# Kernel tuning notes

Measured on AMD Instinct MI355X. Metric: run time of the kernel, lower is better.

Reference implementation:

```python
import jax, jax.numpy as jnp
import numpy as np

B, N, D_IN, D, H, L, K = 64, 1024, 16, 256, 4, 3, 64
DH = D // H
DFF = 4 * D
TAU = 0.5


def setup_inputs() -> dict:
    key = jax.random.key(0)
    ks = jax.random.split(key, 24)
    nrm = lambda k, s: jax.random.normal(k, s, jnp.float32) * 0.02
    u = jax.random.uniform(ks[1], (B, N), jnp.float32, 1e-6, 1.0 - 1e-6)
    return {
        "x": jax.random.normal(ks[0], (B, N, D_IN), jnp.float32),
        "gumbel": -jnp.log(-jnp.log(u)),
        "emb_W": nrm(ks[2], (D_IN, D)), "emb_b": jnp.zeros((D,), jnp.float32),
        "Wq": nrm(ks[3], (L, D, D)), "Wk": nrm(ks[4], (L, D, D)),
        "Wv": nrm(ks[5], (L, D, D)), "Wo": nrm(ks[6], (L, D, D)),
        "ln1_g": jnp.ones((L, D), jnp.float32), "ln1_b": jnp.zeros((L, D), jnp.float32),
        "ln2_g": jnp.ones((L, D), jnp.float32), "ln2_b": jnp.zeros((L, D), jnp.float32),
        "ffn_W1": nrm(ks[7], (L, D, DFF)), "ffn_b1": jnp.zeros((L, DFF), jnp.float32),
        "ffn_W2": nrm(ks[8], (L, DFF, D)), "ffn_b2": jnp.zeros((L, D), jnp.float32),
        "sha_Wq": nrm(ks[9], (D, D)), "sha_Wk": nrm(ks[10], (D, D)),
        "alloc_W1": nrm(ks[11], (D, D)), "alloc_b1": jnp.zeros((D,), jnp.float32),
        "alloc_W2": nrm(ks[12], (D, N)), "alloc_b2": jnp.zeros((N,), jnp.float32),
    }


def _ln(x, g, b):
    m = x.mean(-1, keepdims=True)
    v = ((x - m) ** 2).mean(-1, keepdims=True)
    return (x - m) * jax.lax.rsqrt(v + 1e-5) * g + b


def reference(x, gumbel, emb_W, emb_b, Wq, Wk, Wv, Wo, ln1_g, ln1_b, ln2_g, ln2_b,
              ffn_W1, ffn_b1, ffn_W2, ffn_b2, sha_Wq, sha_Wk,
              alloc_W1, alloc_b1, alloc_W2, alloc_b2):
    h = x @ emb_W + emb_b  # [B,N,D]
    scale = 1.0 / jnp.sqrt(jnp.float32(DH))
    for i in range(L):  # fixed small layer count
        q = (h @ Wq[i]).reshape(B, N, H, DH)
        k = (h @ Wk[i]).reshape(B, N, H, DH)
        v = (h @ Wv[i]).reshape(B, N, H, DH)
        attn = jax.nn.softmax(jnp.einsum('bqhd,bkhd->bhqk', q, k) * scale, axis=-1)
        o = jnp.einsum('bhqk,bkhd->bqhd', attn, v).reshape(B, N, D) @ Wo[i]
        h = _ln(h + o, ln1_g[i], ln1_b[i])
        f = jax.nn.relu(h @ ffn_W1[i] + ffn_b1[i]) @ ffn_W2[i] + ffn_b2[i]
        h = _ln(h + f, ln2_g[i], ln2_b[i])
    h_mean = h.mean(axis=1)  # [B,D]
    qv = h_mean @ sha_Wq  # [B,D]
    kv = h @ sha_Wk       # [B,N,D]
    scores = jnp.einsum('bd,bnd->bn', qv, kv) / jnp.sqrt(jnp.float32(D))  # [B,N]
    weights = jax.nn.softmax((scores + gumbel) / TAU, axis=-1)  # gumbel-softmax, hard=False
    topk_vals, topk_idx = jax.lax.top_k(weights, K)
    logits = jax.nn.relu(h_mean @ alloc_W1 + alloc_b1) @ alloc_W2 + alloc_b2  # [B,N]
    alloc = jax.nn.softmax(logits, axis=-1)
    sel = jnp.take_along_axis(alloc, topk_idx, axis=1)  # [B,K]
    sel = sel / (sel.sum(axis=1, keepdims=True) + 1e-12)
    return weights, topk_idx, sel
```

## Files before the change

kernel.cpp:

```cpp
#include <hip/hip_runtime.h>
#include <math.h>

#define BB   64
#define NN   1024
#define DIN  16
#define DD   256
#define HH   4
#define LL   3
#define DHH  64
#define DFF2 1024
#define KSEL 64

__global__ __launch_bounds__(256) void embed_kernel(
    const float* __restrict__ x, const float* __restrict__ W,
    const float* __restrict__ bias, float* __restrict__ h)
{
  __shared__ float xs[4][DIN];
  const int t = threadIdx.x, w = t >> 6, lane = t & 63;
  const size_t row = (size_t)blockIdx.x * 4 + w;
  if (lane < DIN) xs[w][lane] = x[row * DIN + lane];
  __syncthreads();
#pragma unroll
  for (int j = 0; j < 4; ++j) {
    const int col = lane + j * 64;
    float acc = bias[col];
#pragma unroll
    for (int kk = 0; kk < DIN; ++kk) acc = fmaf(xs[w][kk], W[kk * DD + col], acc);
    h[row * DD + col] = acc;
  }
}

__global__ __launch_bounds__(256) void gemm128_kernel(
    const float* __restrict__ A, int lda,
    const float* __restrict__ Bm, int ldb,
    float* C, int ldc,
    const float* __restrict__ bias,
    const float* res, int ldres,
    int Kk, int relu, int accum)
{
  __shared__ __align__(16) float As[8][132];
  __shared__ __align__(16) float Bs[8][132];
  const int t = threadIdx.x;
  const int tx = t & 15, ty = t >> 4;
  const size_t row0 = (size_t)blockIdx.y * 128;
  const size_t col0 = (size_t)blockIdx.x * 128;
  const int arow = t >> 1, aq = (t & 1) * 4;
  const int brow = t >> 5, bcq = t & 31;
  const int bphys = ((bcq >> 1) | ((bcq & 1) << 4)) * 4;
  float acc[8][8] = {};
  const float* Aptr = A + (row0 + arow) * lda + aq;
  const float* Bptr = Bm + (size_t)brow * ldb + col0 + bcq * 4;

  for (int k0 = 0; k0 < Kk; k0 += 8) {
    const float4 av = *(const float4*)(Aptr + k0);
    const float4 bv = *(const float4*)(Bptr + (size_t)k0 * ldb);
    As[aq + 0][arow] = av.x; As[aq + 1][arow] = av.y;
    As[aq + 2][arow] = av.z; As[aq + 3][arow] = av.w;
    *(float4*)&Bs[brow][bphys] = bv;
    __syncthreads();
#pragma unroll
    for (int kk = 0; kk < 8; ++kk) {
      const float4 a0 = *(const float4*)&As[kk][ty * 8];
      const float4 a1 = *(const float4*)&As[kk][ty * 8 + 4];
      const float4 b0 = *(const float4*)&Bs[kk][tx * 4];
      const float4 b1 = *(const float4*)&Bs[kk][tx * 4 + 64];
      const float aa[8] = {a0.x, a0.y, a0.z, a0.w, a1.x, a1.y, a1.z, a1.w};
      const float bb2[8] = {b0.x, b0.y, b0.z, b0.w, b1.x, b1.y, b1.z, b1.w};
#pragma unroll
      for (int i = 0; i < 8; ++i)
#pragma unroll
        for (int j = 0; j < 8; ++j)
          acc[i][j] = fmaf(aa[i], bb2[j], acc[i][j]);
    }
    __syncthreads();
  }
#pragma unroll
  for (int i = 0; i < 8; ++i) {
    const size_t r = row0 + ty * 8 + i;
    float* cp = C + r * (size_t)ldc + col0 + tx * 8;
    const float* rp = res ? res + r * (size_t)ldres + col0 + tx * 8 : nullptr;
#pragma unroll
    for (int j = 0; j < 8; ++j) {
      const size_t c = col0 + tx * 8 + j;
      float v = acc[i][j];
      if (bias) v += bias[c];
      if (rp)   v += rp[j];
      if (relu) v = fmaxf(v, 0.f);
      if (accum) v += cp[j];
      cp[j] = v;
    }
  }
}

#define TOFF(r, cq) ((r) * 68 + 4 * ((cq) ^ (((r) >> 2) & 15)))

__global__ __launch_bounds__(256) void attn_kernel(
    const float* __restrict__ qb, const float* __restrict__ kb,
    const float* __restrict__ vb, float* __restrict__ ob)
{
  __shared__ __align__(16) float Qn[64 * 68];
  __shared__ __align__(16) float KV[64 * 68];
  __shared__ __align__(16) float Pt[64 * 68];
  const int t = threadIdx.x;
  const int tx = t & 15, ty = t >> 4;
  const int qt = blockIdx.x, hh = blockIdx.y, b = blockIdx.z;
  const size_t base = ((size_t)b * NN) * DD + (size_t)hh * DHH;

  const int srow = t >> 4, scq = t & 15;

  {
    const float* qp = qb + base + (size_t)(qt * 64) * DD + scq * 4;
    const float* kp = kb + base + scq * 4;
#pragma unroll
    for (int u = 0; u < 4; ++u) {
      const int r = srow + 16 * u;
      *(float4*)&Qn[TOFF(r, scq)] = *(const float4*)(qp + (size_t)r * DD);
      *(float4*)&KV[TOFF(r, scq)] = *(const float4*)(kp + (size_t)r * DD);
    }
  }

  float S[4][4], O[4][4] = {}, mrun[4], lrun[4] = {};
#pragma unroll
  for (int i = 0; i < 4; ++i) mrun[i] = -1e30f;

  for (int kt = 0; kt < 16; ++kt) {
    __syncthreads();

    float4 vreg[4];
    {
      const float* vp = vb + base + (size_t)(kt * 64) * DD + scq * 4;
#pragma unroll
      for (int u = 0; u < 4; ++u)
        vreg[u] = *(const float4*)(vp + (size_t)(srow + 16 * u) * DD);
    }

#pragma unroll
    for (int i = 0; i < 4; ++i)
#pragma unroll
      for (int j = 0; j < 4; ++j) S[i][j] = 0.f;
#pragma unroll
    for (int dq = 0; dq < 16; ++dq) {
      float4 q4[4], k4[4];
#pragma unroll
      for (int ii = 0; ii < 4; ++ii) q4[ii] = *(const float4*)&Qn[TOFF(4 * ty + ii, dq)];
#pragma unroll
      for (int jj = 0; jj < 4; ++jj) k4[jj] = *(const float4*)&KV[TOFF(4 * tx + jj, dq)];
#pragma unroll
      for (int ii = 0; ii < 4; ++ii)
#pragma unroll
        for (int jj = 0; jj < 4; ++jj)
          S[ii][jj] += q4[ii].x * k4[jj].x + q4[ii].y * k4[jj].y +
                       q4[ii].z * k4[jj].z + q4[ii].w * k4[jj].w;
    }

    float alpha[4];
#pragma unroll
    for (int ii = 0; ii < 4; ++ii) {
      float mt = -1e30f;
#pragma unroll
      for (int jj = 0; jj < 4; ++jj) { S[ii][jj] *= 0.125f; mt = fmaxf(mt, S[ii][jj]); }
#pragma unroll
      for (int off = 1; off < 16; off <<= 1) mt = fmaxf(mt, __shfl_xor(mt, off));
      const float mnew = fmaxf(mrun[ii], mt);
      alpha[ii] = __expf(mrun[ii] - mnew);
      mrun[ii] = mnew;
      float rs = 0.f;
#pragma unroll
      for (int jj = 0; jj < 4; ++jj) { S[ii][jj] = __expf(S[ii][jj] - mnew); rs += S[ii][jj]; }
#pragma unroll
      for (int off = 1; off < 16; off <<= 1) rs += __shfl_xor(rs, off);
      lrun[ii] = lrun[ii] * alpha[ii] + rs;
    }
#pragma unroll
    for (int jj = 0; jj < 4; ++jj) {
      float4 pv = {S[0][jj], S[1][jj], S[2][jj], S[3][jj]};
      *(float4*)&Pt[TOFF(4 * tx + jj, ty)] = pv;
    }

    __syncthreads();

#pragma unroll
    for (int u = 0; u < 4; ++u)
      *(float4*)&KV[TOFF(srow + 16 * u, scq)] = vreg[u];

    float4 kreg[4];
    {
      const int ktn = (kt + 1) & 15;
      const float* kp = kb + base + (size_t)(ktn * 64) * DD + scq * 4;
#pragma unroll
      for (int u = 0; u < 4; ++u)
        kreg[u] = *(const float4*)(kp + (size_t)(srow + 16 * u) * DD);
    }

    __syncthreads();

#pragma unroll
    for (int ii = 0; ii < 4; ++ii)
#pragma unroll
      for (int jj = 0; jj < 4; ++jj) O[ii][jj] *= alpha[ii];
#pragma unroll
    for (int c = 0; c < 64; ++c) {
      const float4 p4 = *(const float4*)&Pt[TOFF(c, ty)];
      const float4 v4 = *(const float4*)&KV[TOFF(c, tx)];
      const float pp[4] = {p4.x, p4.y, p4.z, p4.w};
      const float vv[4] = {v4.x, v4.y, v4.z, v4.w};
#pragma unroll
      for (int ii = 0; ii < 4; ++ii)
#pragma unroll
        for (int jj = 0; jj < 4; ++jj)
          O[ii][jj] = fmaf(pp[ii], vv[jj], O[ii][jj]);
    }

    __syncthreads();

#pragma unroll
    for (int u = 0; u < 4; ++u)
      *(float4*)&KV[TOFF(srow + 16 * u, scq)] = kreg[u];
  }

#pragma unroll
  for (int ii = 0; ii < 4; ++ii) {
    const float inv = 1.f / lrun[ii];
    float4 o4 = {O[ii][0] * inv, O[ii][1] * inv, O[ii][2] * inv, O[ii][3] * inv};
    *(float4*)(ob + base + (size_t)(qt * 64 + 4 * ty + ii) * DD + 4 * tx) = o4;
  }
}

__global__ __launch_bounds__(256) void ln_kernel(
    const float* in, float* out,
    const float* __restrict__ g, const float* __restrict__ bb)
{
  const int t = threadIdx.x, w = t >> 6, lane = t & 63;
  const size_t row = (size_t)blockIdx.x * 4 + w;
  const float4 val = *(const float4*)(in + row * DD + lane * 4);
  float s = val.x + val.y + val.z + val.w;
#pragma unroll
  for (int off = 32; off; off >>= 1) s += __shfl_xor(s, off);
  const float mean = s * (1.f / 256.f);
  const float dx = val.x - mean, dy = val.y - mean, dz = val.z - mean, dw = val.w - mean;
  float ss = dx * dx + dy * dy + dz * dz + dw * dw;
#pragma unroll
  for (int off = 32; off; off >>= 1) ss += __shfl_xor(ss, off);
  const float inv = rsqrtf(ss * (1.f / 256.f) + 1e-5f);
  const float4 g4 = *(const float4*)(g + lane * 4);
  const float4 b4 = *(const float4*)(bb + lane * 4);
  float4 o4;
  o4.x = dx * inv * g4.x + b4.x;
  o4.y = dy * inv * g4.y + b4.y;
  o4.z = dz * inv * g4.z + b4.z;
  o4.w = dw * inv * g4.w + b4.w;
  *(float4*)(out + row * DD + lane * 4) = o4;
}

__global__ __launch_bounds__(256) void rowmean_kernel(
    const float* __restrict__ h, float* __restrict__ hm)
{
  const int t = threadIdx.x, b = blockIdx.x;
  const float* p = h + (size_t)b * NN * DD + t;
  float acc = 0.f;
  for (int n = 0; n < NN; ++n) acc += p[(size_t)n * DD];
  hm[b * DD + t] = acc * (1.f / NN);
}

__global__ __launch_bounds__(256) void final_small_kernel(
    const float* __restrict__ hm, const float* __restrict__ shaWq,
    const float* __restrict__ W1, const float* __restrict__ b1,
    const float* __restrict__ W2, const float* __restrict__ b2,
    float* __restrict__ qv, float* __restrict__ allocp)
{
  __shared__ float hs[256];
  __shared__ float mids[256];
  __shared__ float red[256];
  const int t = threadIdx.x, b = blockIdx.x;
  hs[t] = hm[b * 256 + t];
  __syncthreads();
  float a = 0.f, m2 = b1[t];
  for (int kk = 0; kk < 256; ++kk) {
    const float hv = hs[kk];
    a  = fmaf(hv, shaWq[kk * 256 + t], a);
    m2 = fmaf(hv, W1[kk * 256 + t], m2);
  }
  qv[b * 256 + t] = a;
  mids[t] = fmaxf(m2, 0.f);
  __syncthreads();
  float lg[4];
#pragma unroll
  for (int j = 0; j < 4; ++j) {
    const int n = t + j * 256;
    float acc2 = b2[n];
    for (int kk = 0; kk < 256; ++kk) acc2 = fmaf(mids[kk], W2[kk * 1024 + n], acc2);
    lg[j] = acc2;
  }
  float m = fmaxf(fmaxf(lg[0], lg[1]), fmaxf(lg[2], lg[3]));
  red[t] = m; __syncthreads();
  for (int s2 = 128; s2; s2 >>= 1) { if (t < s2) red[t] = fmaxf(red[t], red[t + s2]); __syncthreads(); }
  m = red[0]; __syncthreads();
  float e[4]; float ls = 0.f;
#pragma unroll
  for (int j = 0; j < 4; ++j) { e[j] = expf(lg[j] - m); ls += e[j]; }
  red[t] = ls; __syncthreads();
  for (int s2 = 128; s2; s2 >>= 1) { if (t < s2) red[t] += red[t + s2]; __syncthreads(); }
  const float invs = 1.f / red[0];
#pragma unroll
  for (int j = 0; j < 4; ++j) allocp[(size_t)b * 1024 + t + j * 256] = e[j] * invs;
}

__global__ __launch_bounds__(256) void scores_kernel(
    const float* __restrict__ qv, const float* __restrict__ kv,
    const float* __restrict__ gum, float* __restrict__ outW,
    float* __restrict__ wcopy)
{
  __shared__ __align__(16) float qs[256];
  __shared__ float sc[1024];
  __shared__ float red[256];
  const int t = threadIdx.x, b = blockIdx.x;
  const int w = t >> 6, lane = t & 63;
  qs[t] = qv[b * 256 + t];
  __syncthreads();
  const float4 myq = *(const float4*)&qs[lane * 4];
  for (int n = w; n < 1024; n += 4) {
    const float4 k4 = *(const float4*)(kv + ((size_t)b * 1024 + n) * 256 + lane * 4);
    float d = myq.x * k4.x + myq.y * k4.y + myq.z * k4.z + myq.w * k4.w;
#pragma unroll
    for (int off = 32; off; off >>= 1) d += __shfl_xor(d, off);
    if (lane == 0) sc[n] = d * (1.f / 16.f);
  }
  __syncthreads();
  float z[4];
#pragma unroll
  for (int j = 0; j < 4; ++j) {
    const int n = t + j * 256;
    z[j] = (sc[n] + gum[(size_t)b * 1024 + n]) * 2.0f;
  }
  float m = fmaxf(fmaxf(z[0], z[1]), fmaxf(z[2], z[3]));
  red[t] = m; __syncthreads();
  for (int s2 = 128; s2; s2 >>= 1) { if (t < s2) red[t] = fmaxf(red[t], red[t + s2]); __syncthreads(); }
  m = red[0]; __syncthreads();
  float e[4]; float ls = 0.f;
#pragma unroll
  for (int j = 0; j < 4; ++j) { e[j] = expf(z[j] - m); ls += e[j]; }
  red[t] = ls; __syncthreads();
  for (int s2 = 128; s2; s2 >>= 1) { if (t < s2) red[t] += red[t + s2]; __syncthreads(); }
  const float invs = 1.f / red[0];
#pragma unroll
  for (int j = 0; j < 4; ++j) {
    const int n = t + j * 256;
    const float wv = e[j] * invs;
    outW[(size_t)b * 1024 + n] = wv;
    wcopy[(size_t)b * 1024 + n] = wv;
  }
}

__global__ __launch_bounds__(256) void topk_kernel(
    const float* __restrict__ wcopy, const float* __restrict__ allocp,
    float* __restrict__ outI, float* __restrict__ outS)
{
  __shared__ float wv[1024];
  __shared__ float rv[4];
  __shared__ int   ri[4];
  __shared__ int   sel[64];
  const int t = threadIdx.x, b = blockIdx.x;
  const int w = t >> 6, lane = t & 63;
#pragma unroll
  for (int j = 0; j < 4; ++j) wv[t * 4 + j] = wcopy[(size_t)b * 1024 + t * 4 + j];
  __syncthreads();
  for (int it = 0; it < 64; ++it) {
    float bv = -1.f; int bi = 1 << 20;
#pragma unroll
    for (int j = 0; j < 4; ++j) {
      const int n = t * 4 + j;
      const float v2 = wv[n];
      if (v2 > bv || (v2 == bv && n < bi)) { bv = v2; bi = n; }
    }
#pragma unroll
    for (int off = 32; off; off >>= 1) {
      const float ov = __shfl_xor(bv, off);
      const int   oi = __shfl_xor(bi, off);
      if (ov > bv || (ov == bv && oi < bi)) { bv = ov; bi = oi; }
    }
    if (lane == 0) { rv[w] = bv; ri[w] = bi; }
    __syncthreads();
    if (t == 0) {
      float B2 = rv[0]; int I2 = ri[0];
      for (int u = 1; u < 4; ++u)
        if (rv[u] > B2 || (rv[u] == B2 && ri[u] < I2)) { B2 = rv[u]; I2 = ri[u]; }
      sel[it] = I2;
      wv[I2] = -1.f;
    }
    __syncthreads();
  }
  if (t < 64) {
    const int idx = sel[t];
    const float sv = allocp[(size_t)b * 1024 + idx];
    float ssum = sv;
#pragma unroll
    for (int off = 32; off; off >>= 1) ssum += __shfl_xor(ssum, off);
    outI[b * 64 + t] = (float)idx;
    outS[b * 64 + t] = sv / (ssum + 1e-12f);
  }
}

extern "C" void kernel_launch(void* const* d_in, const int* in_sizes, int n_in,
                              void* d_out, int out_size, void* d_ws, size_t ws_size,
                              hipStream_t stream)
{
  (void)in_sizes; (void)n_in; (void)out_size; (void)ws_size;
  const float* x      = (const float*)d_in[0];
  const float* gumbel = (const float*)d_in[1];
  const float* emb_W  = (const float*)d_in[2];
  const float* emb_b  = (const float*)d_in[3];
  const float* Wq     = (const float*)d_in[4];
  const float* Wk     = (const float*)d_in[5];
  const float* Wv     = (const float*)d_in[6];
  const float* Wo     = (const float*)d_in[7];
  const float* ln1_g  = (const float*)d_in[8];
  const float* ln1_b  = (const float*)d_in[9];
  const float* ln2_g  = (const float*)d_in[10];
  const float* ln2_b  = (const float*)d_in[11];
  const float* ffn_W1 = (const float*)d_in[12];
  const float* ffn_b1 = (const float*)d_in[13];
  const float* ffn_W2 = (const float*)d_in[14];
  const float* ffn_b2 = (const float*)d_in[15];
  const float* sha_Wq = (const float*)d_in[16];
  const float* sha_Wk = (const float*)d_in[17];
  const float* aW1    = (const float*)d_in[18];
  const float* ab1    = (const float*)d_in[19];
  const float* aW2    = (const float*)d_in[20];
  const float* ab2    = (const float*)d_in[21];

  float* ws = (float*)d_ws;
  const size_t U = (size_t)BB * NN * DD;
  float* h     = ws;
  float* obuf  = ws + U;
  float* carea = ws + 2 * U;
  const size_t HC = U / 2;
  float* qc = carea;
  float* kc = carea + HC;
  float* vc = carea + 2 * HC;
  float* fbuf = carea;
  float* hmean  = carea;
  float* qvb    = carea + BB * DD;
  float* allocp = carea + 2 * BB * DD;
  float* wcopy  = allocp + (size_t)BB * NN;

  float* outW = (float*)d_out;
  float* outI = outW + (size_t)BB * NN;
  float* outS = outI + BB * KSEL;

  const dim3 blk(256);
  const int M = BB * NN;

  auto GEMM = [&](const float* A, int lda, const float* Bp, int ldb,
                  float* C, int ldc, const float* bias, const float* res,
                  int ldres, int Mm, int Nn, int Kk, int relu, int accum) {
    gemm128_kernel<<<dim3(Nn / 128, Mm / 128), blk, 0, stream>>>(
        A, lda, Bp, ldb, C, ldc, bias, res, ldres, Kk, relu, accum);
  };

  embed_kernel<<<dim3(M / 4), blk, 0, stream>>>(x, emb_W, emb_b, h);

  for (int i = 0; i < LL; ++i) {
    const float* wq  = Wq + (size_t)i * DD * DD;
    const float* wk  = Wk + (size_t)i * DD * DD;
    const float* wvp = Wv + (size_t)i * DD * DD;
    const float* wo  = Wo + (size_t)i * DD * DD;
    const float* w1  = ffn_W1 + (size_t)i * DD * DFF2;
    const float* b1  = ffn_b1 + (size_t)i * DFF2;
    const float* w2  = ffn_W2 + (size_t)i * DFF2 * DD;
    const float* b2  = ffn_b2 + (size_t)i * DD;

    for (int half = 0; half < 2; ++half) {
      const size_t roff = (size_t)half * (M / 2) * DD;
      const int Mc = M / 2;
      GEMM(h + roff, DD, wq,  DD, qc, DD, nullptr, nullptr, 0, Mc, DD, DD, 0, 0);
      GEMM(h + roff, DD, wk,  DD, kc, DD, nullptr, nullptr, 0, Mc, DD, DD, 0, 0);
      GEMM(h + roff, DD, wvp, DD, vc, DD, nullptr, nullptr, 0, Mc, DD, DD, 0, 0);
      attn_kernel<<<dim3(NN / 64, HH, BB / 2), blk, 0, stream>>>(qc, kc, vc, obuf + roff);
    }
    GEMM(obuf, DD, wo, DD, h, DD, nullptr, h, DD, M, DD, DD, 0, 0);
    ln_kernel<<<dim3(M / 4), blk, 0, stream>>>(h, h, ln1_g + i * DD, ln1_b + i * DD);

    for (int c = 0; c < 4; ++c) {
      GEMM(h, DD, w1 + c * 256, DFF2, obuf, 256, b1 + c * 256, nullptr, 0,
           M, 256, DD, 1, 0);
      GEMM(obuf, 256, w2 + (size_t)c * 256 * DD, DD, fbuf, DD,
           (c == 0) ? b2 : nullptr, (c == 0) ? h : nullptr, DD,
           M, DD, 256, 0, (c == 0) ? 0 : 1);
    }
    ln_kernel<<<dim3(M / 4), blk, 0, stream>>>(fbuf, h, ln2_g + i * DD, ln2_b + i * DD);
  }

  rowmean_kernel<<<dim3(BB), blk, 0, stream>>>(h, hmean);
  final_small_kernel<<<dim3(BB), blk, 0, stream>>>(hmean, sha_Wq, aW1, ab1, aW2, ab2, qvb, allocp);
  GEMM(h, DD, sha_Wk, DD, obuf, DD, nullptr, nullptr, 0, M, DD, DD, 0, 0);
  scores_kernel<<<dim3(BB), blk, 0, stream>>>(qvb, obuf, gumbel, outW, wcopy);
  topk_kernel<<<dim3(BB), blk, 0, stream>>>(wcopy, allocp, outI, outS);
}
```

Baseline: 10.85 ms.

## Double-buffer GEMM smem tiles and enlarge attention query tile to 128 rows

The GEMM kernel now uses a K-step of 16 with double-buffered shared-memory tiles. The next tile is prefetched into registers while the current one is computed, which halves the barriers per K element. The attention kernel processes 128 query rows per block instead of 64, so each K/V tile loaded into shared memory is reused across twice as many queries. This costs more registers and shared memory and leaves half as many attention blocks, which may lower occupancy.

```diff
diff --git a/kernel.cpp b/kernel.cpp
--- a/kernel.cpp
+++ b/kernel.cpp
@@ -38,39 +38,66 @@
     const float* res, int ldres,
     int Kk, int relu, int accum)
 {
-  __shared__ __align__(16) float As[8][132];
-  __shared__ __align__(16) float Bs[8][132];
+  __shared__ __align__(16) float As[2][16][132];
+  __shared__ __align__(16) float Bs[2][16][132];
   const int t = threadIdx.x;
   const int tx = t & 15, ty = t >> 4;
   const size_t row0 = (size_t)blockIdx.y * 128;
   const size_t col0 = (size_t)blockIdx.x * 128;
-  const int arow = t >> 1, aq = (t & 1) * 4;
-  const int brow = t >> 5, bcq = t & 31;
-  const int bphys = ((bcq >> 1) | ((bcq & 1) << 4)) * 4;
+  const int arow = t >> 1, ak = (t & 1) * 8;
+  const int brow = t >> 4, bcq = t & 15;
+  const int bp = ((bcq >> 1) | ((bcq & 1) << 4)) * 4;
+  const float* Aptr = A + (row0 + arow) * lda + ak;
+  const float* Bptr = Bm + (size_t)brow * ldb + col0 + bcq * 4;
+
+  float4 a0r, a1r, b0r, b1r;
+  a0r = *(const float4*)(Aptr);
+  a1r = *(const float4*)(Aptr + 4);
+  b0r = *(const float4*)(Bptr);
+  b1r = *(const float4*)(Bptr + 64);
+  {
+    As[0][ak + 0][arow] = a0r.x; As[0][ak + 1][arow] = a0r.y;
+    As[0][ak + 2][arow] = a0r.z; As[0][ak + 3][arow] = a0r.w;
+    As[0][ak + 4][arow] = a1r.x; As[0][ak + 5][arow] = a1r.y;
+    As[0][ak + 6][arow] = a1r.z; As[0][ak + 7][arow] = a1r.w;
+    *(float4*)&Bs[0][brow][bp] = b0r;
+    *(float4*)&Bs[0][brow][bp + 32] = b1r;
+  }
+  __syncthreads();
+
   float acc[8][8] = {};
-  const float* Aptr = A + (row0 + arow) * lda + aq;
-  const float* Bptr = Bm + (size_t)brow * ldb + col0 + bcq * 4;
-
-  for (int k0 = 0; k0 < Kk; k0 += 8) {
-    const float4 av = *(const float4*)(Aptr + k0);
-    const float4 bv = *(const float4*)(Bptr + (size_t)k0 * ldb);
-    As[aq + 0][arow] = av.x; As[aq + 1][arow] = av.y;
-    As[aq + 2][arow] = av.z; As[aq + 3][arow] = av.w;
-    *(float4*)&Bs[brow][bphys] = bv;
-    __syncthreads();
-#pragma unroll
-    for (int kk = 0; kk < 8; ++kk) {
-      const float4 a0 = *(const float4*)&As[kk][ty * 8];
-      const float4 a1 = *(const float4*)&As[kk][ty * 8 + 4];
-      const float4 b0 = *(const float4*)&Bs[kk][tx * 4];
-      const float4 b1 = *(const float4*)&Bs[kk][tx * 4 + 64];
-      const float aa[8] = {a0.x, a0.y, a0.z, a0.w, a1.x, a1.y, a1.z, a1.w};
-      const float bb2[8] = {b0.x, b0.y, b0.z, b0.w, b1.x, b1.y, b1.z, b1.w};
+  const int NT = Kk >> 4;
+  for (int kt = 0; kt < NT; ++kt) {
+    const int cur = kt & 1;
+    if (kt + 1 < NT) {
+      const int k0 = (kt + 1) * 16;
+      a0r = *(const float4*)(Aptr + k0);
+      a1r = *(const float4*)(Aptr + k0 + 4);
+      b0r = *(const float4*)(Bptr + (size_t)k0 * ldb);
+      b1r = *(const float4*)(Bptr + (size_t)k0 * ldb + 64);
+    }
+#pragma unroll
+    for (int kk = 0; kk < 16; ++kk) {
+      const float4 x0 = *(const float4*)&As[cur][kk][ty * 8];
+      const float4 x1 = *(const float4*)&As[cur][kk][ty * 8 + 4];
+      const float4 y0 = *(const float4*)&Bs[cur][kk][tx * 4];
+      const float4 y1 = *(const float4*)&Bs[cur][kk][tx * 4 + 64];
+      const float aa[8] = {x0.x, x0.y, x0.z, x0.w, x1.x, x1.y, x1.z, x1.w};
+      const float bb2[8] = {y0.x, y0.y, y0.z, y0.w, y1.x, y1.y, y1.z, y1.w};
 #pragma unroll
       for (int i = 0; i < 8; ++i)
 #pragma unroll
         for (int j = 0; j < 8; ++j)
           acc[i][j] = fmaf(aa[i], bb2[j], acc[i][j]);
+    }
+    if (kt + 1 < NT) {
+      const int nxt = cur ^ 1;
+      As[nxt][ak + 0][arow] = a0r.x; As[nxt][ak + 1][arow] = a0r.y;
+      As[nxt][ak + 2][arow] = a0r.z; As[nxt][ak + 3][arow] = a0r.w;
+      As[nxt][ak + 4][arow] = a1r.x; As[nxt][ak + 5][arow] = a1r.y;
+      As[nxt][ak + 6][arow] = a1r.z; As[nxt][ak + 7][arow] = a1r.w;
+      *(float4*)&Bs[nxt][brow][bp] = b0r;
+      *(float4*)&Bs[nxt][brow][bp + 32] = b1r;
     }
     __syncthreads();
   }
@@ -92,70 +119,88 @@
   }
 }
 
-#define TOFF(r, cq) ((r) * 68 + 4 * ((cq) ^ (((r) >> 2) & 15)))
+#define TFQ(r, cq) ((r) * 64 + 4 * ((((r) >> 2) ^ (cq)) & 15))
+#define TFP(r, cq) ((r) * 128 + 4 * (((((r) >> 2) & 15) ^ (cq)) & 31))
 
 __global__ __launch_bounds__(256) void attn_kernel(
     const float* __restrict__ qb, const float* __restrict__ kb,
     const float* __restrict__ vb, float* __restrict__ ob)
 {
-  __shared__ __align__(16) float Qn[64 * 68];
-  __shared__ __align__(16) float KV[64 * 68];
-  __shared__ __align__(16) float Pt[64 * 68];
+  __shared__ __align__(16) float Qn[128 * 64];
+  __shared__ __align__(16) float KV[64 * 64];
+  __shared__ __align__(16) float Pt[64 * 128];
   const int t = threadIdx.x;
   const int tx = t & 15, ty = t >> 4;
   const int qt = blockIdx.x, hh = blockIdx.y, b = blockIdx.z;
   const size_t base = ((size_t)b * NN) * DD + (size_t)hh * DHH;
-
   const int srow = t >> 4, scq = t & 15;
 
   {
-    const float* qp = qb + base + (size_t)(qt * 64) * DD + scq * 4;
+    const float* qp = qb + base + (size_t)(qt * 128) * DD + scq * 4;
+#pragma unroll
+    for (int u = 0; u < 8; ++u) {
+      const int r = srow + 16 * u;
+      *(float4*)&Qn[TFQ(r, scq)] = *(const float4*)(qp + (size_t)r * DD);
+    }
     const float* kp = kb + base + scq * 4;
 #pragma unroll
     for (int u = 0; u < 4; ++u) {
       const int r = srow + 16 * u;
-      *(float4*)&Qn[TOFF(r, scq)] = *(const float4*)(qp + (size_t)r * DD);
-      *(float4*)&KV[TOFF(r, scq)] = *(const float4*)(kp + (size_t)r * DD);
-    }
-  }
-
-  float S[4][4], O[4][4] = {}, mrun[4], lrun[4] = {};
-#pragma unroll
-  for (int i = 0; i < 4; ++i) mrun[i] = -1e30f;
+      *(float4*)&KV[TFQ(r, scq)] = *(const float4*)(kp + (size_t)r * DD);
+    }
+  }
+  float4 vreg[4];
+  {
+    const float* vp = vb + base + scq * 4;
+#pragma unroll
+    for (int u = 0; u < 4; ++u)
+      vreg[u] = *(const float4*)(vp + (size_t)(srow + 16 * u) * DD);
+  }
+  __syncthreads();
+
+  const float* qrow[8];
+  const float* krow[4];
+#pragma unroll
+  for (int ii = 0; ii < 4; ++ii) {
+    qrow[ii]     = &Qn[(4 * ty + ii) * 64];
+    qrow[4 + ii] = &Qn[(64 + 4 * ty + ii) * 64];
+    krow[ii]     = &KV[(4 * tx + ii) * 64];
+  }
+
+  float O[8][4] = {}, mrun[8], lrun[8] = {};
+#pragma unroll
+  for (int i = 0; i < 8; ++i) mrun[i] = -1e30f;
 
   for (int kt = 0; kt < 16; ++kt) {
-    __syncthreads();
-
-    float4 vreg[4];
+    float S[8][4] = {};
+#pragma unroll
+    for (int dq = 0; dq < 16; ++dq) {
+      const int xq = 4 * ((dq ^ ty) & 15);
+      const int xk = 4 * ((dq ^ tx) & 15);
+      float4 k4[4];
+#pragma unroll
+      for (int jj = 0; jj < 4; ++jj) k4[jj] = *(const float4*)(krow[jj] + xk);
+#pragma unroll
+      for (int ii = 0; ii < 8; ++ii) {
+        const float4 q4 = *(const float4*)(qrow[ii] + xq);
+#pragma unroll
+        for (int jj = 0; jj < 4; ++jj)
+          S[ii][jj] += q4.x * k4[jj].x + q4.y * k4[jj].y +
+                       q4.z * k4[jj].z + q4.w * k4[jj].w;
+      }
+    }
+
+    float4 kreg[4];
     {
-      const float* vp = vb + base + (size_t)(kt * 64) * DD + scq * 4;
+      const float* kp = kb + base + (size_t)(((kt + 1) & 15) * 64) * DD + scq * 4;
 #pragma unroll
       for (int u = 0; u < 4; ++u)
-        vreg[u] = *(const float4*)(vp + (size_t)(srow + 16 * u) * DD);
-    }
-
-#pragma unroll
-    for (int i = 0; i < 4; ++i)
-#pragma unroll
-      for (int j = 0; j < 4; ++j) S[i][j] = 0.f;
-#pragma unroll
-    for (int dq = 0; dq < 16; ++dq) {
-      float4 q4[4], k4[4];
-#pragma unroll
-      for (int ii = 0; ii < 4; ++ii) q4[ii] = *(const float4*)&Qn[TOFF(4 * ty + ii, dq)];
-#pragma unroll
-      for (int jj = 0; jj < 4; ++jj) k4[jj] = *(const float4*)&KV[TOFF(4 * tx + jj, dq)];
-#pragma unroll
-      for (int ii = 0; ii < 4; ++ii)
-#pragma unroll
-        for (int jj = 0; jj < 4; ++jj)
-          S[ii][jj] += q4[ii].x * k4[jj].x + q4[ii].y * k4[jj].y +
-                       q4[ii].z * k4[jj].z + q4[ii].w * k4[jj].w;
-    }
-
-    float alpha[4];
-#pragma unroll
-    for (int ii = 0; ii < 4; ++ii) {
+        kreg[u] = *(const float4*)(kp + (size_t)(srow + 16 * u) * DD);
+    }
+
+    float alpha[8];
+#pragma unroll
+    for (int ii = 0; ii < 8; ++ii) {
       float mt = -1e30f;
 #pragma unroll
       for (int jj = 0; jj < 4; ++jj) { S[ii][jj] *= 0.125f; mt = fmaxf(mt, S[ii][jj]); }
@@ -171,58 +216,69 @@
       for (int off = 1; off < 16; off <<= 1) rs += __shfl_xor(rs, off);
       lrun[ii] = lrun[ii] * alpha[ii] + rs;
     }
+
+    __syncthreads();
+
+#pragma unroll
+    for (int u = 0; u < 4; ++u)
+      *(float4*)&KV[TFQ(srow + 16 * u, scq)] = vreg[u];
 #pragma unroll
     for (int jj = 0; jj < 4; ++jj) {
-      float4 pv = {S[0][jj], S[1][jj], S[2][jj], S[3][jj]};
-      *(float4*)&Pt[TOFF(4 * tx + jj, ty)] = pv;
+      const float4 plo = {S[0][jj], S[1][jj], S[2][jj], S[3][jj]};
+      const float4 phi = {S[4][jj], S[5][jj], S[6][jj], S[7][jj]};
+      *(float4*)&Pt[TFP(4 * tx + jj, ty)] = plo;
+      *(float4*)&Pt[TFP(4 * tx + jj, 16 + ty)] = phi;
+    }
+
+    __syncthreads();
+
+    {
+      const float* vp = vb + base + (size_t)(((kt + 1) & 15) * 64) * DD + scq * 4;
+#pragma unroll
+      for (int u = 0; u < 4; ++u)
+        vreg[u] = *(const float4*)(vp + (size_t)(srow + 16 * u) * DD);
+    }
+
+#pragma unroll
+    for (int ii = 0; ii < 8; ++ii)
+#pragma unroll
+      for (int jj = 0; jj < 4; ++jj) O[ii][jj] *= alpha[ii];
+#pragma unroll 16
+    for (int c = 0; c < 64; ++c) {
+      const int sc = (c >> 2) & 15;
+      const float4 plo = *(const float4*)&Pt[c * 128 + 4 * (ty ^ sc)];
+      const float4 phi = *(const float4*)&Pt[c * 128 + 4 * ((16 + ty) ^ sc)];
+      const float4 v4  = *(const float4*)&KV[c * 64 + 4 * (tx ^ sc)];
+      const float pl[4] = {plo.x, plo.y, plo.z, plo.w};
+      const float ph[4] = {phi.x, phi.y, phi.z, phi.w};
+#pragma unroll
+      for (int ii = 0; ii < 4; ++ii) {
+        O[ii][0] = fmaf(pl[ii], v4.x, O[ii][0]);
+        O[ii][1] = fmaf(pl[ii], v4.y, O[ii][1]);
+        O[ii][2] = fmaf(pl[ii], v4.z, O[ii][2]);
+        O[ii][3] = fmaf(pl[ii], v4.w, O[ii][3]);
+        O[4 + ii][0] = fmaf(ph[ii], v4.x, O[4 + ii][0]);
+        O[4 + ii][1] = fmaf(ph[ii], v4.y, O[4 + ii][1]);
+        O[4 + ii][2] = fmaf(ph[ii], v4.z, O[4 + ii][2]);
+        O[4 + ii][3] = fmaf(ph[ii], v4.w, O[4 + ii][3]);
+      }
     }
 
     __syncthreads();
 
 #pragma unroll
     for (int u = 0; u < 4; ++u)
-      *(float4*)&KV[TOFF(srow + 16 * u, scq)] = vreg[u];
-
-    float4 kreg[4];
-    {
-      const int ktn = (kt + 1) & 15;
-      const float* kp = kb + base + (size_t)(ktn * 64) * DD + scq * 4;
-#pragma unroll
-      for (int u = 0; u < 4; ++u)
-        kreg[u] = *(const float4*)(kp + (size_t)(srow + 16 * u) * DD);
-    }
-
-    __syncthreads();
-
-#pragma unroll
-    for (int ii = 0; ii < 4; ++ii)
-#pragma unroll
-      for (int jj = 0; jj < 4; ++jj) O[ii][jj] *= alpha[ii];
-#pragma unroll
-    for (int c = 0; c < 64; ++c) {
-      const float4 p4 = *(const float4*)&Pt[TOFF(c, ty)];
-      const float4 v4 = *(const float4*)&KV[TOFF(c, tx)];
-      const float pp[4] = {p4.x, p4.y, p4.z, p4.w};
-      const float vv[4] = {v4.x, v4.y, v4.z, v4.w};
-#pragma unroll
-      for (int ii = 0; ii < 4; ++ii)
-#pragma unroll
-        for (int jj = 0; jj < 4; ++jj)
-          O[ii][jj] = fmaf(pp[ii], vv[jj], O[ii][jj]);
-    }
-
-    __syncthreads();
-
-#pragma unroll
-    for (int u = 0; u < 4; ++u)
-      *(float4*)&KV[TOFF(srow + 16 * u, scq)] = kreg[u];
-  }
-
-#pragma unroll
-  for (int ii = 0; ii < 4; ++ii) {
+      *(float4*)&KV[TFQ(srow + 16 * u, scq)] = kreg[u];
+
+    __syncthreads();
+  }
+
+#pragma unroll
+  for (int ii = 0; ii < 8; ++ii) {
+    const int r = (ii < 4) ? (4 * ty + ii) : (64 + 4 * ty + (ii - 4));
     const float inv = 1.f / lrun[ii];
-    float4 o4 = {O[ii][0] * inv, O[ii][1] * inv, O[ii][2] * inv, O[ii][3] * inv};
-    *(float4*)(ob + base + (size_t)(qt * 64 + 4 * ty + ii) * DD + 4 * tx) = o4;
+    const float4 o4 = {O[ii][0] * inv, O[ii][1] * inv, O[ii][2] * inv, O[ii][3] * inv};
+    *(float4*)(ob + base + (size_t)(qt * 128 + r) * DD + 4 * tx) = o4;
   }
 }
 
@@ -475,7 +531,7 @@
       GEMM(h + roff, DD, wq,  DD, qc, DD, nullptr, nullptr, 0, Mc, DD, DD, 0, 0);
       GEMM(h + roff, DD, wk,  DD, kc, DD, nullptr, nullptr, 0, Mc, DD, DD, 0, 0);
       GEMM(h + roff, DD, wvp, DD, vc, DD, nullptr, nullptr, 0, Mc, DD, DD, 0, 0);
-      attn_kernel<<<dim3(NN / 64, HH, BB / 2), blk, 0, stream>>>(qc, kc, vc, obuf + roff);
+      attn_kernel<<<dim3(NN / 128, HH, BB / 2), blk, 0, stream>>>(qc, kc, vc, obuf + roff);
     }
     GEMM(obuf, DD, wo, DD, h, DD, nullptr, h, DD, M, DD, DD, 0, 0);
     ln_kernel<<<dim3(M / 4), blk, 0, stream>>>(h, h, ln1_g + i * DD, ln1_b + i * DD);
```

Measured after the change: 15.08 ms. 39.1% more time.

## Rework attention to a single 64-thread wave with 8x8 register tiles

Applied to the files above, without the earlier changes.

The flash-attention kernel now runs with one 64-thread wave per block instead of four. Each thread computes an 8x8 tile of scores and outputs rather than 4x4, which raises FMA work per shared-memory read. The per-row softmax rescale factors and running sums move to shared memory, and the V tile is prefetched into registers one step ahead. The GEMM's A tile in shared memory gets a padded stride-12 layout to cut bank conflicts on its float4 reads. The costs are heavy register pressure (S, O and prefetch buffers of 64 values each) and fewer waves per CU, since each block still holds about 52KB of LDS.

```diff
diff --git a/kernel.cpp b/kernel.cpp
--- a/kernel.cpp
+++ b/kernel.cpp
@@ -38,34 +38,34 @@
     const float* res, int ldres,
     int Kk, int relu, int accum)
 {
-  __shared__ __align__(16) float As[8][132];
+  __shared__ __align__(16) float As[8][192];
   __shared__ __align__(16) float Bs[8][132];
   const int t = threadIdx.x;
   const int tx = t & 15, ty = t >> 4;
   const size_t row0 = (size_t)blockIdx.y * 128;
   const size_t col0 = (size_t)blockIdx.x * 128;
   const int arow = t >> 1, aq = (t & 1) * 4;
+  const int acol = 12 * (arow >> 3) + (arow & 7);
   const int brow = t >> 5, bcq = t & 31;
-  const int bphys = ((bcq >> 1) | ((bcq & 1) << 4)) * 4;
+  const int bp = ((bcq >> 1) | ((bcq & 1) << 4)) * 4;
   float acc[8][8] = {};
   const float* Aptr = A + (row0 + arow) * lda + aq;
   const float* Bptr = Bm + (size_t)brow * ldb + col0 + bcq * 4;
-
   for (int k0 = 0; k0 < Kk; k0 += 8) {
     const float4 av = *(const float4*)(Aptr + k0);
     const float4 bv = *(const float4*)(Bptr + (size_t)k0 * ldb);
-    As[aq + 0][arow] = av.x; As[aq + 1][arow] = av.y;
-    As[aq + 2][arow] = av.z; As[aq + 3][arow] = av.w;
-    *(float4*)&Bs[brow][bphys] = bv;
+    As[aq + 0][acol] = av.x; As[aq + 1][acol] = av.y;
+    As[aq + 2][acol] = av.z; As[aq + 3][acol] = av.w;
+    *(float4*)&Bs[brow][bp] = bv;
     __syncthreads();
 #pragma unroll
     for (int kk = 0; kk < 8; ++kk) {
-      const float4 a0 = *(const float4*)&As[kk][ty * 8];
-      const float4 a1 = *(const float4*)&As[kk][ty * 8 + 4];
-      const float4 b0 = *(const float4*)&Bs[kk][tx * 4];
-      const float4 b1 = *(const float4*)&Bs[kk][tx * 4 + 64];
-      const float aa[8] = {a0.x, a0.y, a0.z, a0.w, a1.x, a1.y, a1.z, a1.w};
-      const float bb2[8] = {b0.x, b0.y, b0.z, b0.w, b1.x, b1.y, b1.z, b1.w};
+      const float4 x0 = *(const float4*)&As[kk][ty * 12];
+      const float4 x1 = *(const float4*)&As[kk][ty * 12 + 4];
+      const float4 y0 = *(const float4*)&Bs[kk][tx * 4];
+      const float4 y1 = *(const float4*)&Bs[kk][tx * 4 + 64];
+      const float aa[8] = {x0.x, x0.y, x0.z, x0.w, x1.x, x1.y, x1.z, x1.w};
+      const float bb2[8] = {y0.x, y0.y, y0.z, y0.w, y1.x, y1.y, y1.z, y1.w};
 #pragma unroll
       for (int i = 0; i < 8; ++i)
 #pragma unroll
@@ -92,137 +92,149 @@
   }
 }
 
-#define TOFF(r, cq) ((r) * 68 + 4 * ((cq) ^ (((r) >> 2) & 15)))
-
-__global__ __launch_bounds__(256) void attn_kernel(
+__global__ __launch_bounds__(64) void attn_kernel(
     const float* __restrict__ qb, const float* __restrict__ kb,
     const float* __restrict__ vb, float* __restrict__ ob)
 {
   __shared__ __align__(16) float Qn[64 * 68];
   __shared__ __align__(16) float KV[64 * 68];
   __shared__ __align__(16) float Pt[64 * 68];
+  __shared__ float alphaL[64];
+  __shared__ float lrunL[64];
   const int t = threadIdx.x;
-  const int tx = t & 15, ty = t >> 4;
+  const int A = t >> 3, Bd = t & 7;
   const int qt = blockIdx.x, hh = blockIdx.y, b = blockIdx.z;
   const size_t base = ((size_t)b * NN) * DD + (size_t)hh * DHH;
-
   const int srow = t >> 4, scq = t & 15;
 
   {
     const float* qp = qb + base + (size_t)(qt * 64) * DD + scq * 4;
     const float* kp = kb + base + scq * 4;
 #pragma unroll
-    for (int u = 0; u < 4; ++u) {
-      const int r = srow + 16 * u;
-      *(float4*)&Qn[TOFF(r, scq)] = *(const float4*)(qp + (size_t)r * DD);
-      *(float4*)&KV[TOFF(r, scq)] = *(const float4*)(kp + (size_t)r * DD);
-    }
-  }
-
-  float S[4][4], O[4][4] = {}, mrun[4], lrun[4] = {};
-#pragma unroll
-  for (int i = 0; i < 4; ++i) mrun[i] = -1e30f;
+    for (int u = 0; u < 16; ++u) {
+      const int r = srow + 4 * u;
+      *(float4*)&Qn[r * 68 + scq * 4] = *(const float4*)(qp + (size_t)r * DD);
+      *(float4*)&KV[r * 68 + scq * 4] = *(const float4*)(kp + (size_t)r * DD);
+    }
+  }
+  lrunL[t] = 0.f;
+  float4 vreg[16];
+  {
+    const float* vp = vb + base + scq * 4;
+#pragma unroll
+    for (int u = 0; u < 16; ++u)
+      vreg[u] = *(const float4*)(vp + (size_t)(srow + 4 * u) * DD);
+  }
+  float mrun[8];
+#pragma unroll
+  for (int i = 0; i < 8; ++i) mrun[i] = -1e30f;
+  float O[8][8] = {};
+  __syncthreads();
 
   for (int kt = 0; kt < 16; ++kt) {
-    __syncthreads();
-
-    float4 vreg[4];
+    float S[8][8];
+#pragma unroll
+    for (int i = 0; i < 8; ++i)
+#pragma unroll
+      for (int j = 0; j < 8; ++j) S[i][j] = 0.f;
+#pragma unroll 2
+    for (int dq = 0; dq < 16; ++dq) {
+      float4 k4[8];
+#pragma unroll
+      for (int j = 0; j < 8; ++j)
+        k4[j] = *(const float4*)&KV[(Bd + 8 * j) * 68 + dq * 4];
+#pragma unroll
+      for (int i = 0; i < 8; ++i) {
+        const float4 q4 = *(const float4*)&Qn[(A + 8 * i) * 68 + dq * 4];
+#pragma unroll
+        for (int j = 0; j < 8; ++j)
+          S[i][j] += q4.x * k4[j].x + q4.y * k4[j].y +
+                     q4.z * k4[j].z + q4.w * k4[j].w;
+      }
+    }
+
+#pragma unroll
+    for (int i = 0; i < 8; ++i) {
+      float mt = -1e30f;
+#pragma unroll
+      for (int j = 0; j < 8; ++j) { S[i][j] *= 0.125f; mt = fmaxf(mt, S[i][j]); }
+      mt = fmaxf(mt, __shfl_xor(mt, 1));
+      mt = fmaxf(mt, __shfl_xor(mt, 2));
+      mt = fmaxf(mt, __shfl_xor(mt, 4));
+      const float mnew = fmaxf(mrun[i], mt);
+      const float alpha = __expf(mrun[i] - mnew);
+      mrun[i] = mnew;
+      float rs = 0.f;
+#pragma unroll
+      for (int j = 0; j < 8; ++j) { S[i][j] = __expf(S[i][j] - mnew); rs += S[i][j]; }
+      rs += __shfl_xor(rs, 1);
+      rs += __shfl_xor(rs, 2);
+      rs += __shfl_xor(rs, 4);
+      if (Bd == 0) {
+        alphaL[A + 8 * i] = alpha;
+        lrunL[A + 8 * i] = lrunL[A + 8 * i] * alpha + rs;
+      }
+#pragma unroll
+      for (int j = 0; j < 8; ++j)
+        Pt[(Bd + 8 * j) * 68 + (A + 8 * i)] = S[i][j];
+    }
+    __syncthreads();
+
+#pragma unroll
+    for (int u = 0; u < 16; ++u)
+      *(float4*)&KV[(srow + 4 * u) * 68 + scq * 4] = vreg[u];
+    float4 kreg[16];
     {
-      const float* vp = vb + base + (size_t)(kt * 64) * DD + scq * 4;
-#pragma unroll
-      for (int u = 0; u < 4; ++u)
-        vreg[u] = *(const float4*)(vp + (size_t)(srow + 16 * u) * DD);
-    }
-
-#pragma unroll
-    for (int i = 0; i < 4; ++i)
-#pragma unroll
-      for (int j = 0; j < 4; ++j) S[i][j] = 0.f;
-#pragma unroll
-    for (int dq = 0; dq < 16; ++dq) {
-      float4 q4[4], k4[4];
-#pragma unroll
-      for (int ii = 0; ii < 4; ++ii) q4[ii] = *(const float4*)&Qn[TOFF(4 * ty + ii, dq)];
-#pragma unroll
-      for (int jj = 0; jj < 4; ++jj) k4[jj] = *(const float4*)&KV[TOFF(4 * tx + jj, dq)];
-#pragma unroll
-      for (int ii = 0; ii < 4; ++ii)
-#pragma unroll
-        for (int jj = 0; jj < 4; ++jj)
-          S[ii][jj] += q4[ii].x * k4[jj].x + q4[ii].y * k4[jj].y +
-                       q4[ii].z * k4[jj].z + q4[ii].w * k4[jj].w;
-    }
-
-    float alpha[4];
-#pragma unroll
-    for (int ii = 0; ii < 4; ++ii) {
-      float mt = -1e30f;
-#pragma unroll
-      for (int jj = 0; jj < 4; ++jj) { S[ii][jj] *= 0.125f; mt = fmaxf(mt, S[ii][jj]); }
-#pragma unroll
-      for (int off = 1; off < 16; off <<= 1) mt = fmaxf(mt, __shfl_xor(mt, off));
-      const float mnew = fmaxf(mrun[ii], mt);
-      alpha[ii] = __expf(mrun[ii] - mnew);
-      mrun[ii] = mnew;
-      float rs = 0.f;
-#pragma unroll
-      for (int jj = 0; jj < 4; ++jj) { S[ii][jj] = __expf(S[ii][jj] - mnew); rs += S[ii][jj]; }
-#pragma unroll
-      for (int off = 1; off < 16; off <<= 1) rs += __shfl_xor(rs, off);
-      lrun[ii] = lrun[ii] * alpha[ii] + rs;
-    }
-#pragma unroll
-    for (int jj = 0; jj < 4; ++jj) {
-      float4 pv = {S[0][jj], S[1][jj], S[2][jj], S[3][jj]};
-      *(float4*)&Pt[TOFF(4 * tx + jj, ty)] = pv;
-    }
-
-    __syncthreads();
-
-#pragma unroll
-    for (int u = 0; u < 4; ++u)
-      *(float4*)&KV[TOFF(srow + 16 * u, scq)] = vreg[u];
-
-    float4 kreg[4];
+      const float* kp = kb + base + (size_t)(((kt + 1) & 15) * 64) * DD + scq * 4;
+#pragma unroll
+      for (int u = 0; u < 16; ++u)
+        kreg[u] = *(const float4*)(kp + (size_t)(srow + 4 * u) * DD);
+    }
+    __syncthreads();
+
+#pragma unroll
+    for (int i = 0; i < 8; ++i) {
+      const float al = alphaL[8 * A + i];
+#pragma unroll
+      for (int j = 0; j < 8; ++j) O[i][j] *= al;
+    }
+#pragma unroll 4
+    for (int c = 0; c < 64; ++c) {
+      const float4 p0 = *(const float4*)&Pt[c * 68 + 8 * A];
+      const float4 p1 = *(const float4*)&Pt[c * 68 + 8 * A + 4];
+      const float4 v0 = *(const float4*)&KV[c * 68 + 8 * Bd];
+      const float4 v1 = *(const float4*)&KV[c * 68 + 8 * Bd + 4];
+      const float pp[8] = {p0.x, p0.y, p0.z, p0.w, p1.x, p1.y, p1.z, p1.w};
+      const float vv[8] = {v0.x, v0.y, v0.z, v0.w, v1.x, v1.y, v1.z, v1.w};
+#pragma unroll
+      for (int i = 0; i < 8; ++i)
+#pragma unroll
+        for (int j = 0; j < 8; ++j)
+          O[i][j] = fmaf(pp[i], vv[j], O[i][j]);
+    }
+    __syncthreads();
+
+#pragma unroll
+    for (int u = 0; u < 16; ++u)
+      *(float4*)&KV[(srow + 4 * u) * 68 + scq * 4] = kreg[u];
     {
-      const int ktn = (kt + 1) & 15;
-      const float* kp = kb + base + (size_t)(ktn * 64) * DD + scq * 4;
-#pragma unroll
-      for (int u = 0; u < 4; ++u)
-        kreg[u] = *(const float4*)(kp + (size_t)(srow + 16 * u) * DD);
-    }
-
-    __syncthreads();
-
-#pragma unroll
-    for (int ii = 0; ii < 4; ++ii)
-#pragma unroll
-      for (int jj = 0; jj < 4; ++jj) O[ii][jj] *= alpha[ii];
-#pragma unroll
-    for (int c = 0; c < 64; ++c) {
-      const float4 p4 = *(const float4*)&Pt[TOFF(c, ty)];
-      const float4 v4 = *(const float4*)&KV[TOFF(c, tx)];
-      const float pp[4] = {p4.x, p4.y, p4.z, p4.w};
-      const float vv[4] = {v4.x, v4.y, v4.z, v4.w};
-#pragma unroll
-      for (int ii = 0; ii < 4; ++ii)
-#pragma unroll
-        for (int jj = 0; jj < 4; ++jj)
-          O[ii][jj] = fmaf(pp[ii], vv[jj], O[ii][jj]);
-    }
-
-    __syncthreads();
-
-#pragma unroll
-    for (int u = 0; u < 4; ++u)
-      *(float4*)&KV[TOFF(srow + 16 * u, scq)] = kreg[u];
-  }
-
-#pragma unroll
-  for (int ii = 0; ii < 4; ++ii) {
-    const float inv = 1.f / lrun[ii];
-    float4 o4 = {O[ii][0] * inv, O[ii][1] * inv, O[ii][2] * inv, O[ii][3] * inv};
-    *(float4*)(ob + base + (size_t)(qt * 64 + 4 * ty + ii) * DD + 4 * tx) = o4;
+      const float* vp = vb + base + (size_t)(((kt + 1) & 15) * 64) * DD + scq * 4;
+#pragma unroll
+      for (int u = 0; u < 16; ++u)
+        vreg[u] = *(const float4*)(vp + (size_t)(srow + 4 * u) * DD);
+    }
+    __syncthreads();
+  }
+
+#pragma unroll
+  for (int i = 0; i < 8; ++i) {
+    const int r = 8 * A + i;
+    const float inv = 1.f / lrunL[r];
+    const float4 o0 = {O[i][0] * inv, O[i][1] * inv, O[i][2] * inv, O[i][3] * inv};
+    const float4 o1 = {O[i][4] * inv, O[i][5] * inv, O[i][6] * inv, O[i][7] * inv};
+    float* op = ob + base + (size_t)(qt * 64 + r) * DD + 8 * Bd;
+    *(float4*)op = o0;
+    *(float4*)(op + 4) = o1;
   }
 }
 
@@ -475,7 +487,7 @@
       GEMM(h + roff, DD, wq,  DD, qc, DD, nullptr, nullptr, 0, Mc, DD, DD, 0, 0);
       GEMM(h + roff, DD, wk,  DD, kc, DD, nullptr, nullptr, 0, Mc, DD, DD, 0, 0);
       GEMM(h + roff, DD, wvp, DD, vc, DD, nullptr, nullptr, 0, Mc, DD, DD, 0, 0);
-      attn_kernel<<<dim3(NN / 64, HH, BB / 2), blk, 0, stream>>>(qc, kc, vc, obuf + roff);
+      attn_kernel<<<dim3(NN / 64, HH, BB / 2), dim3(64), 0, stream>>>(qc, kc, vc, obuf + roff);
     }
     GEMM(obuf, DD, wo, DD, h, DD, nullptr, h, DD, M, DD, DD, 0, 0);
     ln_kernel<<<dim3(M / 4), blk, 0, stream>>>(h, h, ln1_g + i * DD, ln1_b + i * DD);
```

Result: slower. 12.16 ms (+12.1%).
